# Kernel optimization log

Measured on AMD Instinct MI355X. Metric: run time of the kernel, lower is better.

The kernel has to match this reference:

```python
import jax, jax.numpy as jnp
import numpy as np

E, B, S, H = 8, 16, 512, 1024
LN_EPS = 1e-12


def setup_inputs() -> dict:
    key = jax.random.key(0)
    k = jax.random.split(key, 5)
    return {
        "hidden_states": jax.random.normal(k[0], (B, S, H), dtype=jnp.float32),
        "input_tensor": jax.random.normal(k[1], (B, S, H), dtype=jnp.float32),
        "expert_idx": jax.random.randint(k[2], (B,), 0, E, dtype=jnp.int64)
        if jax.config.jax_enable_x64 else jax.random.randint(k[2], (B,), 0, E, dtype=jnp.int32),
        "W": jax.random.normal(k[3], (E, H, H), dtype=jnp.float32) * (1.0 / np.sqrt(H)),
        "b": jax.random.normal(k[4], (E, H), dtype=jnp.float32) * 0.02,
        "gamma": jnp.ones((H,), dtype=jnp.float32),
        "beta": jnp.zeros((H,), dtype=jnp.float32),
    }


def reference(hidden_states, input_tensor, expert_idx, W, b, gamma, beta):
    # All-expert dense forward, matching single_select_fwd's stacked compute.
    # all_out: [E, B, S, H]
    all_out = jnp.einsum("bsh,ehd->ebsd", hidden_states, W) + b[:, None, None, :]
    # slice_for_expert: pick (expert_idx[b], b) for each batch row -> [B, S, H]
    selected = all_out[expert_idx, jnp.arange(hidden_states.shape[0])]
    # dropout is identity in eval mode; residual + LayerNorm
    x = selected + input_tensor
    mu = jnp.mean(x, axis=-1, keepdims=True)
    var = jnp.mean(jnp.square(x - mu), axis=-1, keepdims=True)
    return (x - mu) * jax.lax.rsqrt(var + LN_EPS) * gamma + beta
```

## Files before the change

kernel.cpp:

```cpp
#include <hip/hip_runtime.h>
#include <hip/hip_bf16.h>

#define BB 16
#define SS 512
#define HH 1024

typedef __attribute__((ext_vector_type(4))) float f32x4;
typedef __attribute__((ext_vector_type(8))) short bhalf8;

static __device__ __forceinline__ unsigned int pack2(float a, float b) {
    __hip_bfloat162 h = __float22bfloat162_rn(make_float2(a, b));
    union { __hip_bfloat162 h; unsigned int u; } cv;
    cv.h = h;
    return cv.u;
}

__global__ __launch_bounds__(256)
void prep_kernel(const float* __restrict__ W, const float* __restrict__ hid,
                 const int* __restrict__ eidx, unsigned short* __restrict__ Wt,
                 unsigned short* __restrict__ hidb)
{
    int bid = blockIdx.x;
    int t = threadIdx.x;
    if (bid < 2048) {
        __shared__ float lds[32 * 132];
        int e  = bid >> 8;
        bool used = false;
        for (int b = 0; b < BB; ++b) used = used || (eidx[b] == e);
        if (!used) return;
        int rem = bid & 255;
        int kt = rem >> 3, dt = rem & 7;
#pragma unroll
        for (int i = 0; i < 4; ++i) {
            int idx = t + i * 256;
            int row = idx >> 5, col4 = idx & 31;
            float4 v = *(const float4*)(W + ((size_t)e << 20)
                        + (size_t)(kt * 32 + row) * HH + dt * 128 + col4 * 4);
            float* dst = &lds[row * 132 + col4 * 4];
            dst[0] = v.x; dst[1] = v.y; dst[2] = v.z; dst[3] = v.w;
        }
        __syncthreads();
        int d = t >> 1, kh = t & 1;
        unsigned int u[8];
#pragma unroll
        for (int p = 0; p < 8; ++p) {
            float a = lds[(kh * 16 + p * 2)     * 132 + d];
            float b = lds[(kh * 16 + p * 2 + 1) * 132 + d];
            u[p] = pack2(a, b);
        }
        unsigned short* dst = Wt + ((size_t)e << 20)
                            + (size_t)(dt * 128 + d) * HH + kt * 32 + kh * 16;
        *reinterpret_cast<uint4*>(dst)     = make_uint4(u[0], u[1], u[2], u[3]);
        *reinterpret_cast<uint4*>(dst + 8) = make_uint4(u[4], u[5], u[6], u[7]);
    } else {
        int bid2 = bid - 2048;
        int r = bid2 * 2 + (t >> 7);
        int col = (t & 127) * 8;
        const float* src = hid + (size_t)r * HH + col;
        float4 v0 = *(const float4*)(src);
        float4 v1 = *(const float4*)(src + 4);
        uint4 o;
        o.x = pack2(v0.x, v0.y); o.y = pack2(v0.z, v0.w);
        o.z = pack2(v1.x, v1.y); o.w = pack2(v1.z, v1.w);
        *reinterpret_cast<uint4*>(hidb + (size_t)r * HH + col) = o;
    }
}

__global__ __launch_bounds__(256, 2)
void gemm_pure_kernel(const unsigned short* __restrict__ hidb,
                      const int* __restrict__ eidx,
                      const unsigned short* __restrict__ Wt,
                      float* __restrict__ out)
{
    __shared__ char ldsA[4 * 8192];
    __shared__ char ldsW[4 * 8192];

    int bx  = blockIdx.x;
    int swz = (bx & 7) * 64 + (bx >> 3);
    int bt   = swz >> 5;
    int tile = swz & 31;
    int mt = tile >> 3, nt = tile & 7;
    int e = eidx[bt];

    int t = threadIdx.x, wave = t >> 6, lane = t & 63;
    int l15 = lane & 15, g = lane >> 4;
    int wm = wave >> 1, wn = wave & 1;

    int brow = bt * SS + mt * 128;
    int ncol0 = nt * 128;

    const unsigned short* asrc[2];
    const unsigned short* wsrc[2];
    int coff[2];
#pragma unroll
    for (int i = 0; i < 2; ++i) {
        int c = t + i * 256;
        int line = c >> 3, p = c & 7, q = p ^ (line & 7);
        int row = line * 2 + (q >> 2), s = q & 3;
        asrc[i] = hidb + (size_t)(brow + row) * HH + s * 8;
        wsrc[i] = Wt + ((size_t)e << 20) + (size_t)(ncol0 + row) * HH + s * 8;
        coff[i] = c * 16;
    }

    auto stage = [&](int ks, int b) {
#pragma unroll
        for (int i = 0; i < 2; ++i)
            __builtin_amdgcn_global_load_lds(
                (const __attribute__((address_space(1))) void*)(asrc[i] + ks * 32),
                (__attribute__((address_space(3))) void*)(ldsA + b * 8192 + coff[i]),
                16, 0, 0);
#pragma unroll
        for (int i = 0; i < 2; ++i)
            __builtin_amdgcn_global_load_lds(
                (const __attribute__((address_space(1))) void*)(wsrc[i] + ks * 32),
                (__attribute__((address_space(3))) void*)(ldsW + b * 8192 + coff[i]),
                16, 0, 0);
    };

    f32x4 acc[4][4] = {};

    auto compute = [&](int b) {
        const char* Af = ldsA + b * 8192;
        const char* Wf = ldsW + b * 8192;
        bhalf8 af[4], bf[4];
#pragma unroll
        for (int mf = 0; mf < 4; ++mf) {
            int r = wm * 64 + mf * 16 + l15;
            int line = r >> 1;
            int p = (g + ((r & 1) << 2)) ^ (line & 7);
            af[mf] = *reinterpret_cast<const bhalf8*>(Af + line * 128 + p * 16);
        }
#pragma unroll
        for (int nf = 0; nf < 4; ++nf) {
            int d = wn * 64 + nf * 16 + l15;
            int line = d >> 1;
            int p = (g + ((d & 1) << 2)) ^ (line & 7);
            bf[nf] = *reinterpret_cast<const bhalf8*>(Wf + line * 128 + p * 16);
        }
        __builtin_amdgcn_s_setprio(1);
#pragma unroll
        for (int mf = 0; mf < 4; ++mf)
#pragma unroll
            for (int nf = 0; nf < 4; ++nf)
                acc[mf][nf] = __builtin_amdgcn_mfma_f32_16x16x32_bf16(
                    af[mf], bf[nf], acc[mf][nf], 0, 0, 0);
        __builtin_amdgcn_s_setprio(0);
    };

    stage(0, 0); stage(1, 1); stage(2, 2);

    for (int ks = 0; ks < 30; ++ks) {
        asm volatile("s_waitcnt vmcnt(8)\n\ts_barrier" ::: "memory");
        if (ks <= 28) stage(ks + 3, (ks + 3) & 3);
        compute(ks & 3);
    }
    asm volatile("s_waitcnt vmcnt(4)\n\ts_barrier" ::: "memory");
    compute(2);
    asm volatile("s_waitcnt vmcnt(0)\n\ts_barrier" ::: "memory");
    compute(3);

#pragma unroll
    for (int nf = 0; nf < 4; ++nf) {
        int dcol = ncol0 + wn * 64 + nf * 16 + l15;
#pragma unroll
        for (int mf = 0; mf < 4; ++mf)
#pragma unroll
            for (int j = 0; j < 4; ++j) {
                int srow = brow + wm * 64 + mf * 16 + g * 4 + j;
                out[(size_t)srow * HH + dcol] = acc[mf][nf][j];
            }
    }
}

__global__ __launch_bounds__(256)
void post_kernel(float* __restrict__ y, const float* __restrict__ inp,
                 const int* __restrict__ eidx, const float* __restrict__ bias,
                 const float* __restrict__ gamma, const float* __restrict__ beta)
{
    int bid = blockIdx.x;
    int row = ((bid & 7) << 10) | (bid >> 3);
    int bt = row >> 9;
    int e = eidx[bt];
    int t = threadIdx.x;

    size_t base = (size_t)row * HH + t * 4;
    float4 v  = *reinterpret_cast<const float4*>(&y[base]);
    float4 iv = *reinterpret_cast<const float4*>(&inp[base]);
    float4 bv = *reinterpret_cast<const float4*>(&bias[e * HH + t * 4]);
    float4 x;
    x.x = v.x + iv.x + bv.x;
    x.y = v.y + iv.y + bv.y;
    x.z = v.z + iv.z + bv.z;
    x.w = v.w + iv.w + bv.w;

    float s1 = x.x + x.y + x.z + x.w;
    float s2 = x.x * x.x + x.y * x.y + x.z * x.z + x.w * x.w;
#pragma unroll
    for (int off = 32; off > 0; off >>= 1) {
        s1 += __shfl_xor(s1, off, 64);
        s2 += __shfl_xor(s2, off, 64);
    }
    __shared__ float red[8];
    if ((t & 63) == 0) { red[(t >> 6) * 2] = s1; red[(t >> 6) * 2 + 1] = s2; }
    __syncthreads();
    float S1 = red[0] + red[2] + red[4] + red[6];
    float S2 = red[1] + red[3] + red[5] + red[7];
    float mu  = S1 * (1.0f / HH);
    float var = S2 * (1.0f / HH) - mu * mu;
    float rs = rsqrtf(var + 1e-12f);

    float4 gv = *reinterpret_cast<const float4*>(&gamma[t * 4]);
    float4 be = *reinterpret_cast<const float4*>(&beta[t * 4]);
    float4 o;
    o.x = (x.x - mu) * rs * gv.x + be.x;
    o.y = (x.y - mu) * rs * gv.y + be.y;
    o.z = (x.z - mu) * rs * gv.z + be.z;
    o.w = (x.w - mu) * rs * gv.w + be.w;
    *reinterpret_cast<float4*>(&y[base]) = o;
}

extern "C" void kernel_launch(void* const* d_in, const int* in_sizes, int n_in,
                              void* d_out, int out_size, void* d_ws, size_t ws_size,
                              hipStream_t stream) {
    const float* hid   = (const float*)d_in[0];
    const float* inp   = (const float*)d_in[1];
    const int*   eidx  = (const int*)d_in[2];
    const float* W     = (const float*)d_in[3];
    const float* bias  = (const float*)d_in[4];
    const float* gamma = (const float*)d_in[5];
    const float* beta  = (const float*)d_in[6];
    float* out = (float*)d_out;

    unsigned short* Wt   = (unsigned short*)d_ws;
    unsigned short* hidb = (unsigned short*)((char*)d_ws + (16u << 20));

    prep_kernel<<<6144, 256, 0, stream>>>(W, hid, eidx, Wt, hidb);
    gemm_pure_kernel<<<512, 256, 0, stream>>>(hidb, eidx, Wt, out);
    post_kernel<<<BB * SS, 256, 0, stream>>>(out, inp, eidx, bias, gamma, beta);
}
```

Measured before the change: 63.15 us.

## Use 256x128 GEMM tiles with 8 waves and restructure the pipeline barriers

The GEMM now runs 512-thread blocks that each compute a 256-row by 128-column tile, so every staged W tile is shared by twice as many rows and W traffic per output drops. The main loop is rearranged so each step reads its fragments from LDS, then issues the next stage's global-to-LDS loads, then hits a barrier before the MFMAs. The aim is to overlap load issue with compute and to cut LDS and global traffic per FLOP. The cost is half as many blocks (256) on a chip with many CUs, more LDS per block (96KB), and the 2-blocks-per-CU launch bound with 512 threads, which may limit occupancy.

```diff
diff --git a/kernel.cpp b/kernel.cpp
--- a/kernel.cpp
+++ b/kernel.cpp
@@ -66,19 +66,19 @@
     }
 }
 
-__global__ __launch_bounds__(256, 2)
-void gemm_pure_kernel(const unsigned short* __restrict__ hidb,
-                      const int* __restrict__ eidx,
-                      const unsigned short* __restrict__ Wt,
-                      float* __restrict__ out)
+__global__ __launch_bounds__(512, 2)
+void gemm8_kernel(const unsigned short* __restrict__ hidb,
+                  const int* __restrict__ eidx,
+                  const unsigned short* __restrict__ Wt,
+                  float* __restrict__ out)
 {
-    __shared__ char ldsA[4 * 8192];
+    __shared__ char ldsA[4 * 16384];
     __shared__ char ldsW[4 * 8192];
 
     int bx  = blockIdx.x;
-    int swz = (bx & 7) * 64 + (bx >> 3);
-    int bt   = swz >> 5;
-    int tile = swz & 31;
+    int swz = (bx & 7) * 32 + (bx >> 3);
+    int bt   = swz >> 4;
+    int tile = swz & 15;
     int mt = tile >> 3, nt = tile & 7;
     int e = eidx[bt];
 
@@ -86,20 +86,26 @@
     int l15 = lane & 15, g = lane >> 4;
     int wm = wave >> 1, wn = wave & 1;
 
-    int brow = bt * SS + mt * 128;
+    int brow = bt * SS + mt * 256;
     int ncol0 = nt * 128;
 
     const unsigned short* asrc[2];
-    const unsigned short* wsrc[2];
-    int coff[2];
+    int aoff[2];
 #pragma unroll
     for (int i = 0; i < 2; ++i) {
-        int c = t + i * 256;
+        int c = t + i * 512;
         int line = c >> 3, p = c & 7, q = p ^ (line & 7);
         int row = line * 2 + (q >> 2), s = q & 3;
         asrc[i] = hidb + (size_t)(brow + row) * HH + s * 8;
-        wsrc[i] = Wt + ((size_t)e << 20) + (size_t)(ncol0 + row) * HH + s * 8;
-        coff[i] = c * 16;
+        aoff[i] = c * 16;
+    }
+    const unsigned short* wsrc;
+    int woff;
+    {
+        int line = t >> 3, p = t & 7, q = p ^ (line & 7);
+        int row = line * 2 + (q >> 2), s = q & 3;
+        wsrc = Wt + ((size_t)e << 20) + (size_t)(ncol0 + row) * HH + s * 8;
+        woff = t * 16;
     }
 
     auto stage = [&](int ks, int b) {
@@ -107,21 +113,19 @@
         for (int i = 0; i < 2; ++i)
             __builtin_amdgcn_global_load_lds(
                 (const __attribute__((address_space(1))) void*)(asrc[i] + ks * 32),
-                (__attribute__((address_space(3))) void*)(ldsA + b * 8192 + coff[i]),
+                (__attribute__((address_space(3))) void*)(ldsA + b * 16384 + aoff[i]),
                 16, 0, 0);
-#pragma unroll
-        for (int i = 0; i < 2; ++i)
-            __builtin_amdgcn_global_load_lds(
-                (const __attribute__((address_space(1))) void*)(wsrc[i] + ks * 32),
-                (__attribute__((address_space(3))) void*)(ldsW + b * 8192 + coff[i]),
-                16, 0, 0);
+        __builtin_amdgcn_global_load_lds(
+            (const __attribute__((address_space(1))) void*)(wsrc + ks * 32),
+            (__attribute__((address_space(3))) void*)(ldsW + b * 8192 + woff),
+            16, 0, 0);
     };
 
     f32x4 acc[4][4] = {};
 
-    auto compute = [&](int b) {
-        const char* Af = ldsA + b * 8192;
-        const char* Wf = ldsW + b * 8192;
+    auto body = [&](int ks, bool do_stage) {
+        const char* Af = ldsA + (ks & 3) * 16384;
+        const char* Wf = ldsW + (ks & 3) * 8192;
         bhalf8 af[4], bf[4];
 #pragma unroll
         for (int mf = 0; mf < 4; ++mf) {
@@ -137,6 +141,8 @@
             int p = (g + ((d & 1) << 2)) ^ (line & 7);
             bf[nf] = *reinterpret_cast<const bhalf8*>(Wf + line * 128 + p * 16);
         }
+        if (do_stage) stage(ks + 3, (ks + 3) & 3);
+        __builtin_amdgcn_s_barrier();
         __builtin_amdgcn_s_setprio(1);
 #pragma unroll
         for (int mf = 0; mf < 4; ++mf)
@@ -148,16 +154,21 @@
     };
 
     stage(0, 0); stage(1, 1); stage(2, 2);
-
-    for (int ks = 0; ks < 30; ++ks) {
-        asm volatile("s_waitcnt vmcnt(8)\n\ts_barrier" ::: "memory");
-        if (ks <= 28) stage(ks + 3, (ks + 3) & 3);
-        compute(ks & 3);
-    }
-    asm volatile("s_waitcnt vmcnt(4)\n\ts_barrier" ::: "memory");
-    compute(2);
-    asm volatile("s_waitcnt vmcnt(0)\n\ts_barrier" ::: "memory");
-    compute(3);
+    asm volatile("s_waitcnt vmcnt(6)" ::: "memory");
+    __builtin_amdgcn_s_barrier();
+
+    for (int ks = 0; ks < 29; ++ks) {
+        body(ks, true);
+        asm volatile("s_waitcnt vmcnt(6)" ::: "memory");
+        __builtin_amdgcn_s_barrier();
+    }
+    body(29, false);
+    asm volatile("s_waitcnt vmcnt(3)" ::: "memory");
+    __builtin_amdgcn_s_barrier();
+    body(30, false);
+    asm volatile("s_waitcnt vmcnt(0)" ::: "memory");
+    __builtin_amdgcn_s_barrier();
+    body(31, false);
 
 #pragma unroll
     for (int nf = 0; nf < 4; ++nf) {
@@ -235,6 +246,6 @@
     unsigned short* hidb = (unsigned short*)((char*)d_ws + (16u << 20));
 
     prep_kernel<<<6144, 256, 0, stream>>>(W, hid, eidx, Wt, hidb);
-    gemm_pure_kernel<<<512, 256, 0, stream>>>(hidb, eidx, Wt, out);
+    gemm8_kernel<<<256, 512, 0, stream>>>(hidb, eidx, Wt, out);
     post_kernel<<<BB * SS, 256, 0, stream>>>(out, inp, eidx, bias, gamma, beta);
 }
```

New measurement: 60.89 us. -3.6%, faster.

## Use triple-buffered LDS pipeline with stage issued after fragment loads

Applied to the files above, without the earlier changes.

Reduces the GEMM's LDS ring from four to three buffers per operand and raises the occupancy hint to three blocks per CU. The next-next K-slice prefetch is now issued after the current fragments are read into registers, with a barrier before the MFMAs so the buffer can be reused safely. This shortens the prefetch distance from three slices to two. It also adds an extra barrier per iteration, in exchange for lower LDS use and potentially higher occupancy.

```diff
diff --git a/kernel.cpp b/kernel.cpp
--- a/kernel.cpp
+++ b/kernel.cpp
@@ -66,14 +66,14 @@
     }
 }
 
-__global__ __launch_bounds__(256, 2)
-void gemm_pure_kernel(const unsigned short* __restrict__ hidb,
-                      const int* __restrict__ eidx,
-                      const unsigned short* __restrict__ Wt,
-                      float* __restrict__ out)
+__global__ __launch_bounds__(256, 3)
+void gemm8_kernel(const unsigned short* __restrict__ hidb,
+                  const int* __restrict__ eidx,
+                  const unsigned short* __restrict__ Wt,
+                  float* __restrict__ out)
 {
-    __shared__ char ldsA[4 * 8192];
-    __shared__ char ldsW[4 * 8192];
+    __shared__ char ldsA[3 * 8192];
+    __shared__ char ldsW[3 * 8192];
 
     int bx  = blockIdx.x;
     int swz = (bx & 7) * 64 + (bx >> 3);
@@ -119,9 +119,9 @@
 
     f32x4 acc[4][4] = {};
 
-    auto compute = [&](int b) {
-        const char* Af = ldsA + b * 8192;
-        const char* Wf = ldsW + b * 8192;
+    auto body = [&](int ks, bool do_stage) {
+        const char* Af = ldsA + (ks % 3) * 8192;
+        const char* Wf = ldsW + (ks % 3) * 8192;
         bhalf8 af[4], bf[4];
 #pragma unroll
         for (int mf = 0; mf < 4; ++mf) {
@@ -137,6 +137,8 @@
             int p = (g + ((d & 1) << 2)) ^ (line & 7);
             bf[nf] = *reinterpret_cast<const bhalf8*>(Wf + line * 128 + p * 16);
         }
+        if (do_stage) stage(ks + 2, (ks + 2) % 3);
+        __builtin_amdgcn_s_barrier();
         __builtin_amdgcn_s_setprio(1);
 #pragma unroll
         for (int mf = 0; mf < 4; ++mf)
@@ -147,17 +149,19 @@
         __builtin_amdgcn_s_setprio(0);
     };
 
-    stage(0, 0); stage(1, 1); stage(2, 2);
+    stage(0, 0); stage(1, 1);
+    asm volatile("s_waitcnt vmcnt(4)" ::: "memory");
+    __builtin_amdgcn_s_barrier();
 
     for (int ks = 0; ks < 30; ++ks) {
-        asm volatile("s_waitcnt vmcnt(8)\n\ts_barrier" ::: "memory");
-        if (ks <= 28) stage(ks + 3, (ks + 3) & 3);
-        compute(ks & 3);
-    }
-    asm volatile("s_waitcnt vmcnt(4)\n\ts_barrier" ::: "memory");
-    compute(2);
-    asm volatile("s_waitcnt vmcnt(0)\n\ts_barrier" ::: "memory");
-    compute(3);
+        body(ks, true);
+        asm volatile("s_waitcnt vmcnt(4)" ::: "memory");
+        __builtin_amdgcn_s_barrier();
+    }
+    body(30, false);
+    asm volatile("s_waitcnt vmcnt(0)" ::: "memory");
+    __builtin_amdgcn_s_barrier();
+    body(31, false);
 
 #pragma unroll
     for (int nf = 0; nf < 4; ++nf) {
@@ -235,6 +239,6 @@
     unsigned short* hidb = (unsigned short*)((char*)d_ws + (16u << 20));
 
     prep_kernel<<<6144, 256, 0, stream>>>(W, hid, eidx, Wt, hidb);
-    gemm_pure_kernel<<<512, 256, 0, stream>>>(hidb, eidx, Wt, out);
+    gemm8_kernel<<<512, 256, 0, stream>>>(hidb, eidx, Wt, out);
     post_kernel<<<BB * SS, 256, 0, stream>>>(out, inp, eidx, bias, gamma, beta);
 }
```

New measurement: 60.55 us. 4.1% less time.
